# Kernel optimization log

Hardware: AMD Instinct MI355X
Metric: run time of the kernel (lower is better)

Reference implementation:

```python
import jax, jax.numpy as jnp
from jax import lax
import numpy as np

NUM_HEAD = 12
EPS = 1e-5            # torch LayerNorm default
NEG_INF = 1.0e12      # self.inf_value in the source
LEAKY_SLOPE = 0.01    # torch LeakyReLU default
MASK_FIRST = True     # maskedAtten=True applies only to block 0


def _layer_norm(x, s, b):
    m = jnp.mean(x, axis=-1, keepdims=True)
    v = jnp.var(x, axis=-1, keepdims=True)
    return (x - m) / jnp.sqrt(v + EPS) * s + b


def _forward(x, conv_w, conv_b, pos, ln0_s, ln0_b, Wq, bq, Wk, bk, Wv, bv,
             Wo, bo, ln1_s, ln1_b, W1, b1, W2, b2, proj_w, proj_b):
    B, C, H, W = x.shape
    E = conv_w.shape[0]
    P = conv_w.shape[-1]
    hd = E // NUM_HEAD

    # patch embed: Conv2d(C, E, P, stride=P)
    h = lax.conv_general_dilated(x, conv_w, (P, P), 'VALID',
                                 dimension_numbers=('NCHW', 'OIHW', 'NCHW'))
    h = h + conv_b[None, :, None, None]
    L = h.shape[2] * h.shape[3]
    h = h.reshape(B, E, L).transpose(0, 2, 1) + pos  # (B, L, E)

    causal = jnp.triu(jnp.ones((L, L), dtype=bool), 1)
    n_layers = Wq.shape[0]
    for i in range(n_layers):
        # --- attention block ---
        xn = _layer_norm(h, ln0_s[i], ln0_b[i])
        q = (xn @ Wq[i] + bq[i]).reshape(B, L, NUM_HEAD, hd).transpose(0, 2, 1, 3)
        k = (xn @ Wk[i] + bk[i]).reshape(B, L, NUM_HEAD, hd).transpose(0, 2, 1, 3)
        v = (xn @ Wv[i] + bv[i]).reshape(B, L, NUM_HEAD, hd).transpose(0, 2, 1, 3)
        scores = jnp.einsum('bhqd,bhkd->bhqk', q, k) * (hd ** -0.5)
        if i == 0 and MASK_FIRST:
            scores = jnp.where(causal, -NEG_INF, scores)
        a = jax.nn.softmax(scores, axis=-1)
        o = jnp.einsum('bhqk,bhkd->bhqd', a, v)  # (B, NH, L, hd)
        # faithful to torch source: reshape(bs, l, emb) WITHOUT permuting heads back
        o = o.reshape(B, L, E)
        o = o @ Wo[i] + bo[i]
        h = o + h  # residual onto pre-LN input
        # --- MLP block ---
        xr = _layer_norm(h, ln1_s[i], ln1_b[i])
        m = xr @ W1[i] + b1[i]
        m = jnp.where(m >= 0, m, LEAKY_SLOPE * m)
        m = m @ W2[i] + b2[i]
        h = m + xr  # residual onto post-LN (as in source)

    y = h @ proj_w + proj_b               # (B, L, C*P*P)
    y = y.transpose(0, 2, 1).reshape(B, C, H, W)
    return y


def setup_inputs() -> dict:
    key = jax.random.key(0)
    B, C, H, W = 8, 3, 384, 384
    P, E, NL = 16, 768, 8
    FF = 4 * E
    L = (H // P) * (W // P)  # 576
    CPP = C * P * P          # 768
    s = 0.02
    ks = jax.random.split(key, 24)
    f32 = jnp.float32
    inp = {
        'x': jax.random.normal(ks[0], (B, C, H, W), f32),
        'conv_w': jax.random.normal(ks[1], (E, C, P, P), f32) * s,
        'conv_b': jax.random.normal(ks[2], (E,), f32) * s,
        'pos': jax.random.normal(ks[3], (1, L, E), f32),
        'ln0_s': jnp.ones((NL, E), f32),
        'ln0_b': jnp.zeros((NL, E), f32),
        'Wq': jax.random.normal(ks[4], (NL, E, E), f32) * s,
        'bq': jax.random.normal(ks[5], (NL, E), f32) * s,
        'Wk': jax.random.normal(ks[6], (NL, E, E), f32) * s,
        'bk': jax.random.normal(ks[7], (NL, E), f32) * s,
        'Wv': jax.random.normal(ks[8], (NL, E, E), f32) * s,
        'bv': jax.random.normal(ks[9], (NL, E), f32) * s,
        'Wo': jax.random.normal(ks[10], (NL, E, E), f32) * s,
        'bo': jax.random.normal(ks[11], (NL, E), f32) * s,
        'ln1_s': jnp.ones((NL, E), f32),
        'ln1_b': jnp.zeros((NL, E), f32),
        'W1': jax.random.normal(ks[12], (NL, E, FF), f32) * s,
        'b1': jax.random.normal(ks[13], (NL, FF), f32) * s,
        'W2': jax.random.normal(ks[14], (NL, FF, E), f32) * s,
        'b2': jax.random.normal(ks[15], (NL, E), f32) * s,
        'proj_w': jax.random.normal(ks[16], (E, CPP), f32) * s,
        'proj_b': jax.random.normal(ks[17], (CPP,), f32) * s,
    }
    return inp


def reference(x, conv_w, conv_b, pos, ln0_s, ln0_b, Wq, bq, Wk, bk, Wv, bv,
              Wo, bo, ln1_s, ln1_b, W1, b1, W2, b2, proj_w, proj_b):
    return _forward(x, conv_w, conv_b, pos, ln0_s, ln0_b, Wq, bq, Wk, bk,
                    Wv, bv, Wo, bo, ln1_s, ln1_b, W1, b1, W2, b2,
                    proj_w, proj_b)
```

## Files before the change

### kernel.cpp

```cpp
#include <hip/hip_runtime.h>
#include <hip/hip_bf16.h>
#include <stdint.h>

#define NLAYERS 8
#define LSEQ 576
#define EMB 768
#define NHEAD 12
#define HDIM 64
#define FFDIM 3072
#define BLROWS 4608

typedef __attribute__((ext_vector_type(8))) short short8;
typedef __attribute__((ext_vector_type(4))) float floatx4;

__device__ __forceinline__ float b2f(short s) {
    union { float f; uint32_t u; } x; x.u = ((uint32_t)(uint16_t)s) << 16; return x.f;
}
__device__ __forceinline__ short f2b(float f) {
    union { float f; uint32_t u; } x; x.f = f;
    uint32_t r = x.u + 0x7fffu + ((x.u >> 16) & 1u);
    return (short)(r >> 16);
}

#define GLDS16(gp, lp) __builtin_amdgcn_global_load_lds( \
    (const __attribute__((address_space(1))) void*)(gp), \
    (__attribute__((address_space(3))) void*)(lp), 16, 0, 0)

__device__ __forceinline__ void xcd_remap(int& bx, int& by) {
    const int gx = gridDim.x;
    const int n  = gx * gridDim.y;
    const int orig = by * gx + bx;
    const int q = n >> 3, r = n & 7;
    const int xcd = orig & 7;
    const int wgid = (xcd < r ? xcd * (q + 1) : r * (q + 1) + (xcd - r) * q) + (orig >> 3);
    bx = wgid % gx;
    by = wgid / gx;
}

template<int MF, bool ADD_POS, bool RES_F32, bool LEAKY, bool OUT_F32>
__global__ __launch_bounds__(256)
void gemm_bt(const short* __restrict__ A, const short* __restrict__ Bt,
             const float* __restrict__ bias, const float* __restrict__ pos,
             const float* __restrict__ resf, void* __restrict__ Cout,
             int N, int K)
{
    constexpr int BM = MF * 32;
    __shared__ short As[BM * 32];
    __shared__ short Bs[128 * 32];
    int bx = blockIdx.x, by = blockIdx.y;
    xcd_remap(bx, by);
    const int t    = threadIdx.x;
    const int lane = t & 63;
    const int w    = t >> 6;
    const int m0   = by * BM;
    const int n0   = bx * 128;
    const int wm   = (w >> 1) * (MF * 16);
    const int wn   = (w & 1) * 64;

    floatx4 acc[MF][4];
#pragma unroll
    for (int i = 0; i < MF; ++i)
#pragma unroll
        for (int j = 0; j < 4; ++j)
            acc[i][j] = (floatx4){0.f, 0.f, 0.f, 0.f};

    const int sr = t >> 2;
    const int sc = (t & 3) * 8;
    const short* Ag = A  + (size_t)(m0 + sr) * K + sc;
    const short* Bg = Bt + (size_t)(n0 + sr) * K + sc;

    for (int k0 = 0; k0 < K; k0 += 32) {
        GLDS16(Ag + k0, &As[(size_t)t * 8]);
        if constexpr (MF == 4)
            GLDS16(Ag + (size_t)64 * K + k0, &As[(size_t)(t + 256) * 8]);
        GLDS16(Bg + k0,                  &Bs[(size_t)t * 8]);
        GLDS16(Bg + (size_t)64 * K + k0, &Bs[(size_t)(t + 256) * 8]);
        __syncthreads();
        short8 af[MF], bf[4];
#pragma unroll
        for (int i = 0; i < MF; ++i)
            af[i] = *(const short8*)&As[(wm + i * 16 + (lane & 15)) * 32 + (lane >> 4) * 8];
#pragma unroll
        for (int j = 0; j < 4; ++j)
            bf[j] = *(const short8*)&Bs[(wn + j * 16 + (lane & 15)) * 32 + (lane >> 4) * 8];
#pragma unroll
        for (int i = 0; i < MF; ++i)
#pragma unroll
            for (int j = 0; j < 4; ++j)
                acc[i][j] = __builtin_amdgcn_mfma_f32_16x16x32_bf16(af[i], bf[j], acc[i][j], 0, 0, 0);
        __syncthreads();
    }

    const int colb = n0 + wn + (lane & 15);
    const int rowb = m0 + wm + ((lane >> 4) * 4);
#pragma unroll
    for (int i = 0; i < MF; ++i) {
#pragma unroll
        for (int j = 0; j < 4; ++j) {
            const int col = colb + j * 16;
            const float bv = bias[col];
#pragma unroll
            for (int r = 0; r < 4; ++r) {
                const int row = rowb + i * 16 + r;
                float v = acc[i][j][r] + bv;
                if constexpr (ADD_POS) v += pos[(size_t)(row % LSEQ) * N + col];
                if constexpr (RES_F32) v += resf[(size_t)row * N + col];
                if constexpr (LEAKY)   v = v >= 0.f ? v : 0.01f * v;
                if constexpr (OUT_F32) ((float*)Cout)[(size_t)row * N + col] = v;
                else                   ((short*)Cout)[(size_t)row * N + col] = f2b(v);
            }
        }
    }
}

__global__ __launch_bounds__(256)
void ln_kernel(const float* __restrict__ h, const float* __restrict__ g,
               const float* __restrict__ bbias, short* __restrict__ outb,
               float* __restrict__ outf)
{
    const int row = blockIdx.x;
    const float* x = h + (size_t)row * EMB;
    const int t = threadIdx.x;
    float v0 = x[t], v1 = x[t + 256], v2 = x[t + 512];
    float s  = v0 + v1 + v2;
    float ss = v0 * v0 + v1 * v1 + v2 * v2;
#pragma unroll
    for (int m = 1; m < 64; m <<= 1) {
        s  += __shfl_xor(s, m, 64);
        ss += __shfl_xor(ss, m, 64);
    }
    __shared__ float red[8];
    if ((t & 63) == 0) { red[t >> 6] = s; red[4 + (t >> 6)] = ss; }
    __syncthreads();
    float S  = red[0] + red[1] + red[2] + red[3];
    float SS = red[4] + red[5] + red[6] + red[7];
    float mean = S * (1.f / 768.f);
    float var  = SS * (1.f / 768.f) - mean * mean;
    float rstd = rsqrtf(var + 1e-5f);
    const size_t base = (size_t)row * EMB;
#pragma unroll
    for (int q = 0; q < 3; ++q) {
        int e = t + q * 256;
        float v = (q == 0 ? v0 : (q == 1 ? v1 : v2));
        float y = (v - mean) * rstd * g[e] + bbias[e];
        outb[base + e] = f2b(y);
        if (outf) outf[base + e] = y;
    }
}

__global__ __launch_bounds__(256)
void repack_kv(const short* __restrict__ qkv, short* __restrict__ kp, short* __restrict__ vt)
{
    const int kt = blockIdx.x, bh = blockIdx.y;
    const int b = bh / 12, h = bh % 12;
    const int t = threadIdx.x;
#pragma unroll
    for (int i = 0; i < 2; ++i) {
        int flat = i * 256 + t;
        int key = flat >> 3, c = flat & 7;
        short8 vK = *(const short8*)(qkv + ((size_t)(b * LSEQ) + kt * 64 + key) * 2304 + 768 + h * 64 + c * 8);
        *(short8*)(kp + ((size_t)bh * LSEQ + kt * 64 + key) * 64 + 8 * (c ^ (key & 7))) = vK;
    }
    __shared__ short tile[64][65];
    const int tx = t & 63, ty = t >> 6;
#pragma unroll
    for (int r = 0; r < 16; ++r) {
        int k = ty * 16 + r;
        tile[k][tx] = qkv[((size_t)(b * LSEQ) + kt * 64 + k) * 2304 + 1536 + h * 64 + tx];
    }
    __syncthreads();
#pragma unroll
    for (int r = 0; r < 16; ++r) {
        int d = ty * 16 + r;
        vt[((size_t)bh * 64 + d) * LSEQ + kt * 64 + (tx ^ ((d & 7) << 3))] = tile[tx][d];
    }
}

__global__ __launch_bounds__(256)
void attn_mfma(const short* __restrict__ qkv, const short* __restrict__ kp,
               const short* __restrict__ vt, short* __restrict__ oout, int causal)
{
    const int qt = blockIdx.x, bh = blockIdx.y;
    const int b = bh / 12, h = bh % 12;
    const int t = threadIdx.x, lane = t & 63, w = t >> 6;

    __shared__ short Ks[64 * 64];
    __shared__ short Vs[64 * 64];
    __shared__ short Plds[4][16][72];

    const int nrow = lane & 15;
    const int kch  = (lane >> 4) * 8;
    const int swz  = (lane & 7) << 3;

    short8 aq[2];
    {
        const short* qrow = qkv + ((size_t)(b * LSEQ) + qt * 64 + w * 16 + nrow) * 2304 + h * 64 + kch;
        aq[0] = *(const short8*)qrow;
        aq[1] = *(const short8*)(qrow + 32);
    }

    float m[4], lsum[4];
    floatx4 oacc[4];
#pragma unroll
    for (int r = 0; r < 4; ++r) { m[r] = -3e38f; lsum[r] = 0.f; }
#pragma unroll
    for (int j = 0; j < 4; ++j) oacc[j] = (floatx4){0.f, 0.f, 0.f, 0.f};

    const int ktend = causal ? qt : 8;
    const short* ksrc = kp + ((size_t)bh * LSEQ) * 64;
    const short* vsrc = vt + ((size_t)bh * 64) * LSEQ;

    for (int kt = 0; kt <= ktend; ++kt) {
        __syncthreads();
        {
            const short* kt_src = ksrc + (size_t)(kt * 64) * 64;
            GLDS16(kt_src + (size_t)t * 8,          &Ks[(size_t)t * 8]);
            GLDS16(kt_src + (size_t)(t + 256) * 8,  &Ks[(size_t)(t + 256) * 8]);
            int f0 = t, f1 = t + 256;
            GLDS16(vsrc + (size_t)(f0 >> 3) * LSEQ + kt * 64 + (f0 & 7) * 8, &Vs[(size_t)f0 * 8]);
            GLDS16(vsrc + (size_t)(f1 >> 3) * LSEQ + kt * 64 + (f1 & 7) * 8, &Vs[(size_t)f1 * 8]);
        }
        __syncthreads();

        floatx4 sc[4];
#pragma unroll
        for (int j = 0; j < 4; ++j) sc[j] = (floatx4){0.f, 0.f, 0.f, 0.f};
#pragma unroll
        for (int s = 0; s < 2; ++s) {
#pragma unroll
            for (int j = 0; j < 4; ++j) {
                short8 bk = *(const short8*)&Ks[(16 * j + nrow) * 64 + ((kch + 32 * s) ^ swz)];
                sc[j] = __builtin_amdgcn_mfma_f32_16x16x32_bf16(aq[s], bk, sc[j], 0, 0, 0);
            }
        }
        float sv[4][4];
#pragma unroll
        for (int j = 0; j < 4; ++j)
#pragma unroll
            for (int r = 0; r < 4; ++r) {
                float v = sc[j][r] * 0.125f;
                if (causal && kt == qt) {
                    int key = kt * 64 + 16 * j + nrow;
                    int qr  = qt * 64 + w * 16 + (lane >> 4) * 4 + r;
                    if (key > qr) v = -1e12f;
                }
                sv[j][r] = v;
            }
#pragma unroll
        for (int r = 0; r < 4; ++r) {
            float tm = fmaxf(fmaxf(sv[0][r], sv[1][r]), fmaxf(sv[2][r], sv[3][r]));
            tm = fmaxf(tm, __shfl_xor(tm, 1, 64));
            tm = fmaxf(tm, __shfl_xor(tm, 2, 64));
            tm = fmaxf(tm, __shfl_xor(tm, 4, 64));
            tm = fmaxf(tm, __shfl_xor(tm, 8, 64));
            float nm = fmaxf(m[r], tm);
            float c  = __expf(m[r] - nm);
            m[r] = nm;
            float ps = 0.f;
#pragma unroll
            for (int j = 0; j < 4; ++j) {
                float p = __expf(sv[j][r] - nm);
                sv[j][r] = p;
                ps += p;
            }
            lsum[r] = lsum[r] * c + ps;
#pragma unroll
            for (int j = 0; j < 4; ++j) oacc[j][r] *= c;
        }
#pragma unroll
        for (int j = 0; j < 4; ++j)
#pragma unroll
            for (int r = 0; r < 4; ++r)
                Plds[w][(lane >> 4) * 4 + r][16 * j + nrow] = f2b(sv[j][r]);
        short8 ap[2];
#pragma unroll
        for (int s = 0; s < 2; ++s)
            ap[s] = *(const short8*)&Plds[w][nrow][kch + 32 * s];
#pragma unroll
        for (int s = 0; s < 2; ++s) {
#pragma unroll
            for (int j = 0; j < 4; ++j) {
                short8 bv = *(const short8*)&Vs[(16 * j + nrow) * 64 + ((kch + 32 * s) ^ swz)];
                oacc[j] = __builtin_amdgcn_mfma_f32_16x16x32_bf16(ap[s], bv, oacc[j], 0, 0, 0);
            }
        }
    }

    float inv[4];
#pragma unroll
    for (int r = 0; r < 4; ++r) {
        float L = lsum[r];
        L += __shfl_xor(L, 1, 64);
        L += __shfl_xor(L, 2, 64);
        L += __shfl_xor(L, 4, 64);
        L += __shfl_xor(L, 8, 64);
        inv[r] = 1.f / L;
    }
#pragma unroll
    for (int j = 0; j < 4; ++j)
#pragma unroll
        for (int r = 0; r < 4; ++r) {
            size_t lq = (size_t)qt * 64 + w * 16 + (lane >> 4) * 4 + r;
            oout[((size_t)bh * LSEQ + lq) * 64 + 16 * j + nrow] = f2b(oacc[j][r] * inv[r]);
        }
}

__global__ void transpose_f2b(const float* __restrict__ in, short* __restrict__ out,
                              int R, int C, long long ibs, long long obs)
{
    __shared__ float tile[32][33];
    const int b = blockIdx.z;
    const float* inb = in + (long long)b * ibs;
    short* outb = out + (long long)b * obs;
    const int r0 = blockIdx.y * 32, c0 = blockIdx.x * 32;
    const int tx = threadIdx.x, ty = threadIdx.y;
#pragma unroll
    for (int i = 0; i < 32; i += 8) tile[ty + i][tx] = inb[(size_t)(r0 + ty + i) * C + c0 + tx];
    __syncthreads();
#pragma unroll
    for (int i = 0; i < 32; i += 8) outb[(size_t)(c0 + ty + i) * R + r0 + tx] = f2b(tile[tx][ty + i]);
}

__global__ void transpose_f2f(const float* __restrict__ in, float* __restrict__ out,
                              int R, int C, long long ibs, long long obs)
{
    __shared__ float tile[32][33];
    const int b = blockIdx.z;
    const float* inb = in + (long long)b * ibs;
    float* outb = out + (long long)b * obs;
    const int r0 = blockIdx.y * 32, c0 = blockIdx.x * 32;
    const int tx = threadIdx.x, ty = threadIdx.y;
#pragma unroll
    for (int i = 0; i < 32; i += 8) tile[ty + i][tx] = inb[(size_t)(r0 + ty + i) * C + c0 + tx];
    __syncthreads();
#pragma unroll
    for (int i = 0; i < 32; i += 8) outb[(size_t)(c0 + ty + i) * R + r0 + tx] = tile[tx][ty + i];
}

__global__ void concat_qkv_bias(const float* __restrict__ bq, const float* __restrict__ bk,
                                const float* __restrict__ bv, float* __restrict__ out)
{
    int i = blockIdx.x * 256 + threadIdx.x;
    int layer = i / 2304, j = i % 2304;
    float v;
    if (j < 768)       v = bq[layer * 768 + j];
    else if (j < 1536) v = bk[layer * 768 + j - 768];
    else               v = bv[layer * 768 + j - 1536];
    out[i] = v;
}

__global__ void im2col_kernel(const float* __restrict__ x, short* __restrict__ xcol)
{
    const size_t idx = (size_t)blockIdx.x * 256 + threadIdx.x;
    const int k = (int)(idx % 768);
    const size_t m = idx / 768;
    const int c  = k >> 8;
    const int ky = (k >> 4) & 15;
    const int kx = k & 15;
    const int b  = (int)(m / 576);
    const int l  = (int)(m % 576);
    const int ph = l / 24, pw = l % 24;
    xcol[idx] = f2b(x[((size_t)(b * 3 + c) * 384 + ph * 16 + ky) * 384 + pw * 16 + kx]);
}

__global__ void cast_f32_b16(const float* __restrict__ in, short* __restrict__ out, int n)
{
    int i = blockIdx.x * 256 + threadIdx.x;
    if (i < n) out[i] = f2b(in[i]);
}

extern "C" void kernel_launch(void* const* d_in, const int* in_sizes, int n_in,
                              void* d_out, int out_size, void* d_ws, size_t ws_size,
                              hipStream_t stream)
{
    const float* x      = (const float*)d_in[0];
    const float* conv_w = (const float*)d_in[1];
    const float* conv_b = (const float*)d_in[2];
    const float* pos    = (const float*)d_in[3];
    const float* ln0_s  = (const float*)d_in[4];
    const float* ln0_b  = (const float*)d_in[5];
    const float* Wq     = (const float*)d_in[6];
    const float* bq     = (const float*)d_in[7];
    const float* Wk     = (const float*)d_in[8];
    const float* bk     = (const float*)d_in[9];
    const float* Wv     = (const float*)d_in[10];
    const float* bv     = (const float*)d_in[11];
    const float* Wo     = (const float*)d_in[12];
    const float* bo     = (const float*)d_in[13];
    const float* ln1_s  = (const float*)d_in[14];
    const float* ln1_b  = (const float*)d_in[15];
    const float* W1     = (const float*)d_in[16];
    const float* b1     = (const float*)d_in[17];
    const float* W2     = (const float*)d_in[18];
    const float* b2     = (const float*)d_in[19];
    const float* proj_w = (const float*)d_in[20];
    const float* proj_b = (const float*)d_in[21];

    char* ws = (char*)d_ws;
    short* qkvT  = (short*)(ws);
    short* woT   = (short*)(ws + 28311552);
    short* w1T   = (short*)(ws + 37748736);
    short* w2T   = (short*)(ws + 75497472);
    short* projT = (short*)(ws + 113246208);
    float* qkvb  = (float*)(ws + 114425856);
    short* tmpA  = (short*)(ws + 114499584);
    float* h     = (float*)(ws + 142811136);
    short* xn    = (short*)(ws + 156966912);
    short* xrb   = (short*)(ws + 164044800);
    float* xrf   = (float*)(ws + 171122688);
    short* qkv   = (short*)(ws + 185278464);
    short* o     = (short*)(ws + 206512128);
    short* convB = (short*)(ws + 213590016);

    short* kp = tmpA;
    short* vt = tmpA + 3538944;

    dim3 tb(32, 8);
    transpose_f2b<<<dim3(24, 24, 8), tb, 0, stream>>>(Wq, qkvT,           768, 768, 589824, 1769472);
    transpose_f2b<<<dim3(24, 24, 8), tb, 0, stream>>>(Wk, qkvT + 589824,  768, 768, 589824, 1769472);
    transpose_f2b<<<dim3(24, 24, 8), tb, 0, stream>>>(Wv, qkvT + 1179648, 768, 768, 589824, 1769472);
    transpose_f2b<<<dim3(24, 24, 8), tb, 0, stream>>>(Wo, woT,            768, 768, 589824, 589824);
    transpose_f2b<<<dim3(96, 24, 8), tb, 0, stream>>>(W1, w1T,            768, 3072, 2359296, 2359296);
    transpose_f2b<<<dim3(24, 96, 8), tb, 0, stream>>>(W2, w2T,            3072, 768, 2359296, 2359296);
    transpose_f2b<<<dim3(24, 24, 1), tb, 0, stream>>>(proj_w, projT,      768, 768, 0, 0);
    cast_f32_b16<<<2304, 256, 0, stream>>>(conv_w, convB, 589824);
    concat_qkv_bias<<<72, 256, 0, stream>>>(bq, bk, bv, qkvb);

    im2col_kernel<<<13824, 256, 0, stream>>>(x, tmpA);
    gemm_bt<2, true, false, false, true><<<dim3(6, 72), 256, 0, stream>>>(
        tmpA, convB, conv_b, pos, nullptr, h, 768, 768);

    for (int i = 0; i < NLAYERS; ++i) {
        ln_kernel<<<4608, 256, 0, stream>>>(h, ln0_s + i * 768, ln0_b + i * 768, xn, nullptr);
        gemm_bt<4, false, false, false, false><<<dim3(18, 36), 256, 0, stream>>>(
            xn, qkvT + (size_t)i * 1769472, qkvb + i * 2304, nullptr, nullptr, qkv, 2304, 768);
        repack_kv<<<dim3(9, 96), 256, 0, stream>>>(qkv, kp, vt);
        attn_mfma<<<dim3(9, 96), 256, 0, stream>>>(qkv, kp, vt, o, i == 0 ? 1 : 0);
        gemm_bt<2, false, true, false, true><<<dim3(6, 72), 256, 0, stream>>>(
            o, woT + (size_t)i * 589824, bo + i * 768, nullptr, h, h, 768, 768);
        ln_kernel<<<4608, 256, 0, stream>>>(h, ln1_s + i * 768, ln1_b + i * 768, xrb, xrf);
        gemm_bt<4, false, false, true, false><<<dim3(24, 36), 256, 0, stream>>>(
            xrb, w1T + (size_t)i * 2359296, b1 + i * 3072, nullptr, nullptr, tmpA, 3072, 768);
        gemm_bt<2, false, true, false, true><<<dim3(6, 72), 256, 0, stream>>>(
            tmpA, w2T + (size_t)i * 2359296, b2 + i * 768, nullptr, xrf, h, 768, 3072);
    }

    short* hb = xn;
    float* yf = (float*)tmpA;
    cast_f32_b16<<<13824, 256, 0, stream>>>(h, hb, 4608 * 768);
    gemm_bt<2, false, false, false, true><<<dim3(6, 72), 256, 0, stream>>>(
        hb, projT, proj_b, nullptr, nullptr, yf, 768, 768);
    transpose_f2f<<<dim3(24, 18, 8), tb, 0, stream>>>(yf, (float*)d_out, 576, 768, 442368, 442368);
}
```

Before: 1.796 ms.

## Double-buffer GEMM LDS tiles with BK=64 and XOR-swizzled layout

Rewrites the bf16 GEMM main loop to use two LDS buffers, so the next K=64 slab is prefetched with global_load_lds while MFMAs run on the current one. The K-tile grows from 32 to 64 and an XOR swizzle on 16-byte chunks is meant to avoid LDS bank conflicts. The MF=4 (128-row) variant is dropped, so the QKV and W1 GEMMs now use 64-row tiles with twice as many blocks. The goal is to hide global latency and halve the barriers per K step, at the cost of more LDS per block and less reuse of B tiles for the large GEMMs.

```diff
diff --git a/kernel.cpp b/kernel.cpp
--- a/kernel.cpp
+++ b/kernel.cpp
@@ -37,64 +37,89 @@
     by = wgid / gx;
 }
 
-template<int MF, bool ADD_POS, bool RES_F32, bool LEAKY, bool OUT_F32>
+template<bool ADD_POS, bool RES_F32, bool LEAKY, bool OUT_F32>
 __global__ __launch_bounds__(256)
 void gemm_bt(const short* __restrict__ A, const short* __restrict__ Bt,
              const float* __restrict__ bias, const float* __restrict__ pos,
              const float* __restrict__ resf, void* __restrict__ Cout,
              int N, int K)
 {
-    constexpr int BM = MF * 32;
-    __shared__ short As[BM * 32];
-    __shared__ short Bs[128 * 32];
+    __shared__ short As[2 * 64 * 64];
+    __shared__ short Bs[2 * 128 * 64];
     int bx = blockIdx.x, by = blockIdx.y;
     xcd_remap(bx, by);
     const int t    = threadIdx.x;
     const int lane = t & 63;
     const int w    = t >> 6;
-    const int m0   = by * BM;
+    const int m0   = by * 64;
     const int n0   = bx * 128;
-    const int wm   = (w >> 1) * (MF * 16);
+    const int wm   = (w >> 1) * 32;
     const int wn   = (w & 1) * 64;
 
-    floatx4 acc[MF][4];
-#pragma unroll
-    for (int i = 0; i < MF; ++i)
+    floatx4 acc[2][4];
+#pragma unroll
+    for (int i = 0; i < 2; ++i)
 #pragma unroll
         for (int j = 0; j < 4; ++j)
             acc[i][j] = (floatx4){0.f, 0.f, 0.f, 0.f};
 
-    const int sr = t >> 2;
-    const int sc = (t & 3) * 8;
-    const short* Ag = A  + (size_t)(m0 + sr) * K + sc;
-    const short* Bg = Bt + (size_t)(n0 + sr) * K + sc;
-
-    for (int k0 = 0; k0 < K; k0 += 32) {
-        GLDS16(Ag + k0, &As[(size_t)t * 8]);
-        if constexpr (MF == 4)
-            GLDS16(Ag + (size_t)64 * K + k0, &As[(size_t)(t + 256) * 8]);
-        GLDS16(Bg + k0,                  &Bs[(size_t)t * 8]);
-        GLDS16(Bg + (size_t)64 * K + k0, &Bs[(size_t)(t + 256) * 8]);
+    const int srow = t >> 3;
+    const int sch  = t & 7;
+
+    const short* Ag = A  + (size_t)m0 * K;
+    const short* Bg = Bt + (size_t)n0 * K;
+
+#define STAGE(buf, k0)                                                              \
+    {                                                                               \
+        _Pragma("unroll")                                                           \
+        for (int i = 0; i < 2; ++i) {                                               \
+            int row = srow + i * 32;                                                \
+            GLDS16(Ag + (size_t)row * K + (k0) + ((sch ^ (row & 7)) << 3),          \
+                   &As[(buf) * 4096 + (size_t)(t + i * 256) * 8]);                  \
+        }                                                                           \
+        _Pragma("unroll")                                                           \
+        for (int i = 0; i < 4; ++i) {                                               \
+            int row = srow + i * 32;                                                \
+            GLDS16(Bg + (size_t)row * K + (k0) + ((sch ^ (row & 7)) << 3),          \
+                   &Bs[(buf) * 8192 + (size_t)(t + i * 256) * 8]);                  \
+        }                                                                           \
+    }
+
+    STAGE(0, 0);
+    __syncthreads();
+    int cur = 0;
+    for (int k0 = 0; k0 < K; k0 += 64) {
+        if (k0 + 64 < K) STAGE(cur ^ 1, k0 + 64);
+#pragma unroll
+        for (int ks = 0; ks < 2; ++ks) {
+            short8 af[2], bf[4];
+#pragma unroll
+            for (int i = 0; i < 2; ++i) {
+                int row = wm + i * 16 + (lane & 15);
+                int ch  = (ks * 4 + (lane >> 4)) ^ (row & 7);
+                af[i] = *(const short8*)&As[cur * 4096 + row * 64 + ch * 8];
+            }
+#pragma unroll
+            for (int j = 0; j < 4; ++j) {
+                int row = wn + j * 16 + (lane & 15);
+                int ch  = (ks * 4 + (lane >> 4)) ^ (row & 7);
+                bf[j] = *(const short8*)&Bs[cur * 8192 + row * 64 + ch * 8];
+            }
+#pragma unroll
+            for (int i = 0; i < 2; ++i)
+#pragma unroll
+                for (int j = 0; j < 4; ++j)
+                    acc[i][j] = __builtin_amdgcn_mfma_f32_16x16x32_bf16(af[i], bf[j], acc[i][j], 0, 0, 0);
+        }
         __syncthreads();
-        short8 af[MF], bf[4];
-#pragma unroll
-        for (int i = 0; i < MF; ++i)
-            af[i] = *(const short8*)&As[(wm + i * 16 + (lane & 15)) * 32 + (lane >> 4) * 8];
-#pragma unroll
-        for (int j = 0; j < 4; ++j)
-            bf[j] = *(const short8*)&Bs[(wn + j * 16 + (lane & 15)) * 32 + (lane >> 4) * 8];
-#pragma unroll
-        for (int i = 0; i < MF; ++i)
-#pragma unroll
-            for (int j = 0; j < 4; ++j)
-                acc[i][j] = __builtin_amdgcn_mfma_f32_16x16x32_bf16(af[i], bf[j], acc[i][j], 0, 0, 0);
-        __syncthreads();
-    }
+        cur ^= 1;
+    }
+#undef STAGE
 
     const int colb = n0 + wn + (lane & 15);
     const int rowb = m0 + wm + ((lane >> 4) * 4);
 #pragma unroll
-    for (int i = 0; i < MF; ++i) {
+    for (int i = 0; i < 2; ++i) {
 #pragma unroll
         for (int j = 0; j < 4; ++j) {
             const int col = colb + j * 16;
@@ -427,28 +452,28 @@
     concat_qkv_bias<<<72, 256, 0, stream>>>(bq, bk, bv, qkvb);
 
     im2col_kernel<<<13824, 256, 0, stream>>>(x, tmpA);
-    gemm_bt<2, true, false, false, true><<<dim3(6, 72), 256, 0, stream>>>(
+    gemm_bt<true, false, false, true><<<dim3(6, 72), 256, 0, stream>>>(
         tmpA, convB, conv_b, pos, nullptr, h, 768, 768);
 
     for (int i = 0; i < NLAYERS; ++i) {
         ln_kernel<<<4608, 256, 0, stream>>>(h, ln0_s + i * 768, ln0_b + i * 768, xn, nullptr);
-        gemm_bt<4, false, false, false, false><<<dim3(18, 36), 256, 0, stream>>>(
+        gemm_bt<false, false, false, false><<<dim3(18, 72), 256, 0, stream>>>(
             xn, qkvT + (size_t)i * 1769472, qkvb + i * 2304, nullptr, nullptr, qkv, 2304, 768);
         repack_kv<<<dim3(9, 96), 256, 0, stream>>>(qkv, kp, vt);
         attn_mfma<<<dim3(9, 96), 256, 0, stream>>>(qkv, kp, vt, o, i == 0 ? 1 : 0);
-        gemm_bt<2, false, true, false, true><<<dim3(6, 72), 256, 0, stream>>>(
+        gemm_bt<false, true, false, true><<<dim3(6, 72), 256, 0, stream>>>(
             o, woT + (size_t)i * 589824, bo + i * 768, nullptr, h, h, 768, 768);
         ln_kernel<<<4608, 256, 0, stream>>>(h, ln1_s + i * 768, ln1_b + i * 768, xrb, xrf);
-        gemm_bt<4, false, false, true, false><<<dim3(24, 36), 256, 0, stream>>>(
+        gemm_bt<false, false, true, false><<<dim3(24, 72), 256, 0, stream>>>(
             xrb, w1T + (size_t)i * 2359296, b1 + i * 3072, nullptr, nullptr, tmpA, 3072, 768);
-        gemm_bt<2, false, true, false, true><<<dim3(6, 72), 256, 0, stream>>>(
+        gemm_bt<false, true, false, true><<<dim3(6, 72), 256, 0, stream>>>(
             tmpA, w2T + (size_t)i * 2359296, b2 + i * 768, nullptr, xrf, h, 768, 3072);
     }
 
     short* hb = xn;
     float* yf = (float*)tmpA;
     cast_f32_b16<<<13824, 256, 0, stream>>>(h, hb, 4608 * 768);
-    gemm_bt<2, false, false, false, true><<<dim3(6, 72), 256, 0, stream>>>(
+    gemm_bt<false, false, false, true><<<dim3(6, 72), 256, 0, stream>>>(
         hb, projT, proj_b, nullptr, nullptr, yf, 768, 768);
     transpose_f2f<<<dim3(24, 18, 8), tb, 0, stream>>>(yf, (float*)d_out, 576, 768, 442368, 442368);
 }
```

Result: faster. 1.695 ms (-5.6%).
